# Kernel tuning notes

Measured on AMD Instinct MI355X. Metric: run time of the kernel, lower is better.

The kernel has to match this reference:

```python
import jax, jax.numpy as jnp
import numpy as np

EPS_XVAR = 1e-06
EPS_QVAR = 1e-05
EPS_VAR = 1e-05
MIN_SCALE = 0.1  # rbf kernel
EPS_EDGE = 1e-06


def setup_inputs() -> dict:
    key = jax.random.key(0)
    k1, k2, k3, k4 = jax.random.split(key, 4)
    B, O, I, M = 2048, 64, 64, 32
    x = jax.random.normal(k1, (B, I), dtype=jnp.float32)
    # inducing locations: linspace(-1.5, 1.5, M) tiled over (O, I)
    z = jnp.broadcast_to(jnp.linspace(-1.5, 1.5, M, dtype=jnp.float32), (O, I, M))
    q_mu = jax.random.normal(k2, (O, I, M), dtype=jnp.float32) * 0.05
    q_log_var = jnp.full((O, I, M), -3.0, dtype=jnp.float32)
    log_scale = jnp.zeros((O, I), dtype=jnp.float32)
    log_variance = jnp.full((O, I), -1.0, dtype=jnp.float32)
    return {"x": x, "z": z, "q_mu": q_mu, "q_log_var": q_log_var,
            "log_scale": log_scale, "log_variance": log_variance}


def reference(x, z, q_mu, q_log_var, log_scale, log_variance):
    # x: [B, I]; params: [O, I, M] or [O, I]
    x_mean = x
    x_var = jnp.zeros_like(x) + EPS_XVAR

    q_var = jnp.maximum(jnp.exp(q_log_var), EPS_QVAR)           # [O, I, M]
    var_kern = jnp.maximum(jnp.exp(log_variance), EPS_VAR)      # [O, I]
    lengthscale = jnp.maximum(jnp.exp(log_scale), MIN_SCALE)    # [O, I]

    x_mu_exp = x_mean[:, None, :, None]        # [B, 1, I, 1]
    x_var_exp = x_var[:, None, :, None]        # [B, 1, I, 1]
    ell_sq = (lengthscale ** 2)[None, :, :, None]  # [1, O, I, 1]
    vk = var_kern[None, :, :, None]            # [1, O, I, 1]

    denom = ell_sq + x_var_exp                 # [B, O, I, 1]
    diff = x_mu_exp - z[None]                  # [B, O, I, M]
    psi_1 = vk * jnp.sqrt(ell_sq / denom) * jnp.exp(-0.5 * diff ** 2 / denom)

    edge_means = jnp.sum(psi_1 * q_mu[None], axis=-1)                      # [B, O, I]
    edge_vars = jnp.sum(psi_1 ** 2 * (q_var + q_mu ** 2)[None], axis=-1)   # [B, O, I]
    edge_vars = jnp.maximum(edge_vars - edge_means ** 2, EPS_EDGE)

    return edge_means.sum(axis=2), edge_vars.sum(axis=2)  # each [B, O]
```

## Files before the change

kernel.cpp:

```cpp
#include <hip/hip_runtime.h>

#define BATCH 2048
#define ODIM 64
#define IDIM 64
#define MDIM 32

static constexpr float LOG2E = 1.4426950408889634f;

#if __has_builtin(__builtin_amdgcn_exp2f)
#define EXP2F(x) __builtin_amdgcn_exp2f(x)
#else
#define EXP2F(x) exp2f(x)
#endif

typedef float v2f __attribute__((ext_vector_type(2)));


__global__ __launch_bounds__(256) void prep_kernel(
    const float* __restrict__ z, const float* __restrict__ q_mu,
    const float* __restrict__ q_log_var, const float* __restrict__ log_scale,
    const float* __restrict__ log_variance,
    float4* __restrict__ cmq, float4* __restrict__ aux)
{
    int qt = blockIdx.x * 256 + threadIdx.x;
    int oi = qt >> 4;
    int k  = qt & 15;
    int g  = oi * MDIM + 2 * k;

    float ls   = log_scale[oi];
    float lv   = log_variance[oi];
    float ell  = fmaxf(expf(ls), 0.1f);
    float ell2 = ell * ell;
    float vk   = fmaxf(expf(lv), 1e-5f);
    float denom = ell2 + 1e-6f;
    float A    = vk * sqrtf(ell2 / denom);
    float a    = -0.5f * LOG2E / denom;

    float qm0 = q_mu[g],     qm1 = q_mu[g + 1];
    float qv0 = fmaxf(expf(q_log_var[g]),     1e-5f);
    float qv1 = fmaxf(expf(q_log_var[g + 1]), 1e-5f);
    float zm0 = z[g],        zm1 = z[g + 1];
    float w0  = exp2f(a * zm0 * zm0);
    float w1  = exp2f(a * zm1 * zm1);

    float4 c;
    c.x = A * qm0 * w0;
    c.y = A * A * (qv0 + qm0 * qm0) * w0 * w0;
    c.z = A * qm1 * w1;
    c.w = A * A * (qv1 + qm1 * qm1) * w1 * w1;
    cmq[qt] = c;

    if (k == 0) {
        float z0 = z[oi * MDIM + 0];
        float z1 = z[oi * MDIM + 1];
        float dz = z1 - z0;
        aux[oi] = make_float4(a, -2.0f * a * z0, -2.0f * a * dz, 0.0f);
    }
}

__global__ __launch_bounds__(512, 8) void gpkan_main_kernel(
    const float* __restrict__ x, const float4* __restrict__ cmq,
    const float4* __restrict__ aux, float* __restrict__ out)
{
    const int o     = blockIdx.x & (ODIM - 1);
    const int btile = blockIdx.x >> 6;
    const int tid   = threadIdx.x;
    const int lane  = tid & 63;
    const int wave  = __builtin_amdgcn_readfirstlane(tid >> 6);
    const int b0    = btile * 128 + 2 * lane;
    const int i0    = wave * 8;

    __shared__ float red[2][8][128];

    const float4* pA = (const float4*)(x + (size_t)b0 * IDIM + i0);
    const float4* pB = (const float4*)(x + (size_t)(b0 + 1) * IDIM + i0);
    float4 a0 = pA[0], a1 = pA[1];
    float4 bb0 = pB[0], bb1 = pB[1];

    v2f xv[8];
    xv[0].x = a0.x; xv[0].y = bb0.x;
    xv[1].x = a0.y; xv[1].y = bb0.y;
    xv[2].x = a0.z; xv[2].y = bb0.z;
    xv[3].x = a0.w; xv[3].y = bb0.w;
    xv[4].x = a1.x; xv[4].y = bb1.x;
    xv[5].x = a1.y; xv[5].y = bb1.y;
    xv[6].x = a1.z; xv[6].y = bb1.z;
    xv[7].x = a1.w; xv[7].y = bb1.w;

    const float4* __restrict__ Cb = cmq + ((size_t)o * IDIM + i0) * 16;
    const float4* __restrict__ Ab = aux + o * IDIM + i0;

    v2f emt = {0.f, 0.f};
    v2f evt = {0.f, 0.f};

    #pragma unroll
    for (int ii = 0; ii < 8; ++ii) {
        const float4 Ax = Ab[ii];
        const v2f x2 = xv[ii];

        v2f e1 = {Ax.x, Ax.x}, e2 = {Ax.y, Ax.y}, rc = {Ax.z, Ax.z};

        v2f t = __builtin_elementwise_fma(e1, x2, e2) * x2;
        v2f Eb;
        Eb.x = EXP2F(t.x); Eb.y = EXP2F(t.y);
        v2f ur = rc * x2;
        v2f rr;
        rr.x = EXP2F(ur.x); rr.y = EXP2F(ur.y);

        v2f s = rr * rr;
        v2f u = s * s;

        v2f Pe = {0.f, 0.f}, Po = {0.f, 0.f};
        v2f Qe = {0.f, 0.f}, Qo = {0.f, 0.f};

        const float4* C = Cb + ii * 16;
        #pragma unroll
        for (int k = 15; k >= 0; --k) {
            float4 c = C[k];
            v2f c1e = {c.x, c.x}, c2e = {c.y, c.y};
            v2f c1o = {c.z, c.z}, c2o = {c.w, c.w};
            Pe = __builtin_elementwise_fma(Pe, s, c1e);
            Po = __builtin_elementwise_fma(Po, s, c1o);
            Qe = __builtin_elementwise_fma(Qe, u, c2e);
            Qo = __builtin_elementwise_fma(Qo, u, c2o);
        }

        v2f P = __builtin_elementwise_fma(rr, Po, Pe);
        v2f Q = __builtin_elementwise_fma(s,  Qo, Qe);

        v2f em_i = Eb * P;
        v2f ev_i = (Eb * Eb) * Q;

        v2f eps = {1e-6f, 1e-6f};
        v2f d   = __builtin_elementwise_fma(-em_i, em_i, ev_i);
        evt += __builtin_elementwise_max(d, eps);
        emt += em_i;
    }

    red[0][wave][2 * lane + 0] = emt.x;
    red[0][wave][2 * lane + 1] = emt.y;
    red[1][wave][2 * lane + 0] = evt.x;
    red[1][wave][2 * lane + 1] = evt.y;
    __syncthreads();

    if (tid < 256) {
        const int sel = tid >> 7;
        const int l   = tid & 127;
        float acc = 0.f;
        #pragma unroll
        for (int w = 0; w < 8; ++w) acc += red[sel][w][l];
        const int bb = btile * 128 + l;
        if (sel == 0) out[bb * ODIM + o] = acc;
        else          out[BATCH * ODIM + bb * ODIM + o] = acc;
    }
}

extern "C" void kernel_launch(void* const* d_in, const int* in_sizes, int n_in,
                              void* d_out, int out_size, void* d_ws, size_t ws_size,
                              hipStream_t stream) {
    const float* x            = (const float*)d_in[0];
    const float* z            = (const float*)d_in[1];
    const float* q_mu         = (const float*)d_in[2];
    const float* q_log_var    = (const float*)d_in[3];
    const float* log_scale    = (const float*)d_in[4];
    const float* log_variance = (const float*)d_in[5];
    float* out = (float*)d_out;

    char* ws = (char*)d_ws;
    float4* cmq = (float4*)ws;
    float4* aux = (float4*)(ws + (size_t)ODIM * IDIM * 16 * sizeof(float4));

    prep_kernel<<<dim3(256), dim3(256), 0, stream>>>(
        z, q_mu, q_log_var, log_scale, log_variance, cmq, aux);
    gpkan_main_kernel<<<dim3((BATCH / 128) * ODIM), dim3(512), 0, stream>>>(
        x, cmq, aux, out);
}
```

Before: 81.96 us.

## Fuse parameter prep into main kernel, staging coefficients in LDS

Removes the separate prep kernel and computes the per-(o,i) polynomial coefficients and aux constants inside each main-kernel block, storing them in shared memory. This drops one kernel launch and the workspace round-trip, and the inner loop now reads coefficients from LDS instead of global memory. In exchange, each of the 16 batch tiles per output recomputes the same 64x16 coefficients with expf/exp2 calls. The block also gains about 17 KB of LDS and an extra barrier, which may limit occupancy.

After: 81.75 us. Within noise of the previous version (-0.3%).

```diff
diff --git a/kernel.cpp b/kernel.cpp
--- a/kernel.cpp
+++ b/kernel.cpp
@@ -15,52 +15,11 @@
 
 typedef float v2f __attribute__((ext_vector_type(2)));
 
-
-__global__ __launch_bounds__(256) void prep_kernel(
-    const float* __restrict__ z, const float* __restrict__ q_mu,
-    const float* __restrict__ q_log_var, const float* __restrict__ log_scale,
-    const float* __restrict__ log_variance,
-    float4* __restrict__ cmq, float4* __restrict__ aux)
-{
-    int qt = blockIdx.x * 256 + threadIdx.x;
-    int oi = qt >> 4;
-    int k  = qt & 15;
-    int g  = oi * MDIM + 2 * k;
-
-    float ls   = log_scale[oi];
-    float lv   = log_variance[oi];
-    float ell  = fmaxf(expf(ls), 0.1f);
-    float ell2 = ell * ell;
-    float vk   = fmaxf(expf(lv), 1e-5f);
-    float denom = ell2 + 1e-6f;
-    float A    = vk * sqrtf(ell2 / denom);
-    float a    = -0.5f * LOG2E / denom;
-
-    float qm0 = q_mu[g],     qm1 = q_mu[g + 1];
-    float qv0 = fmaxf(expf(q_log_var[g]),     1e-5f);
-    float qv1 = fmaxf(expf(q_log_var[g + 1]), 1e-5f);
-    float zm0 = z[g],        zm1 = z[g + 1];
-    float w0  = exp2f(a * zm0 * zm0);
-    float w1  = exp2f(a * zm1 * zm1);
-
-    float4 c;
-    c.x = A * qm0 * w0;
-    c.y = A * A * (qv0 + qm0 * qm0) * w0 * w0;
-    c.z = A * qm1 * w1;
-    c.w = A * A * (qv1 + qm1 * qm1) * w1 * w1;
-    cmq[qt] = c;
-
-    if (k == 0) {
-        float z0 = z[oi * MDIM + 0];
-        float z1 = z[oi * MDIM + 1];
-        float dz = z1 - z0;
-        aux[oi] = make_float4(a, -2.0f * a * z0, -2.0f * a * dz, 0.0f);
-    }
-}
-
-__global__ __launch_bounds__(512, 8) void gpkan_main_kernel(
-    const float* __restrict__ x, const float4* __restrict__ cmq,
-    const float4* __restrict__ aux, float* __restrict__ out)
+__global__ __launch_bounds__(512, 8) void gpkan_fused_kernel(
+    const float* __restrict__ x, const float* __restrict__ z,
+    const float* __restrict__ q_mu, const float* __restrict__ q_log_var,
+    const float* __restrict__ log_scale, const float* __restrict__ log_variance,
+    float* __restrict__ out)
 {
     const int o     = blockIdx.x & (ODIM - 1);
     const int btile = blockIdx.x >> 6;
@@ -70,12 +29,52 @@
     const int b0    = btile * 128 + 2 * lane;
     const int i0    = wave * 8;
 
-    __shared__ float red[2][8][128];
+    __shared__ float4 lds_c[IDIM][16];
+    __shared__ float4 lds_aux[IDIM];
+    __shared__ float  red[2][8][128];
 
     const float4* pA = (const float4*)(x + (size_t)b0 * IDIM + i0);
     const float4* pB = (const float4*)(x + (size_t)(b0 + 1) * IDIM + i0);
     float4 a0 = pA[0], a1 = pA[1];
     float4 bb0 = pB[0], bb1 = pB[1];
+
+    #pragma unroll
+    for (int rep = 0; rep < 2; ++rep) {
+        const int q  = tid + rep * 512;
+        const int i  = q >> 4;
+        const int k  = q & 15;
+        const int oi = o * IDIM + i;
+        const int g  = oi * MDIM + 2 * k;
+
+        const float ls = log_scale[oi];
+        const float lv = log_variance[oi];
+        const float ell   = fmaxf(expf(ls), 0.1f);
+        const float ell2  = ell * ell;
+        const float vk    = fmaxf(expf(lv), 1e-5f);
+        const float denom = ell2 + 1e-6f;
+        const float A = vk * sqrtf(ell2 / denom);
+        const float a = -0.5f * LOG2E / denom;
+
+        const float2 qm = *(const float2*)(q_mu + g);
+        const float2 ql = *(const float2*)(q_log_var + g);
+        const float2 zm = *(const float2*)(z + g);
+        const float qv0 = fmaxf(expf(ql.x), 1e-5f);
+        const float qv1 = fmaxf(expf(ql.y), 1e-5f);
+        const float w0  = EXP2F(a * zm.x * zm.x);
+        const float w1  = EXP2F(a * zm.y * zm.y);
+
+        float4 c;
+        c.x = A * qm.x * w0;
+        c.y = A * A * (qv0 + qm.x * qm.x) * w0 * w0;
+        c.z = A * qm.y * w1;
+        c.w = A * A * (qv1 + qm.y * qm.y) * w1 * w1;
+        lds_c[i][k] = c;
+
+        if (k == 0)
+            lds_aux[i] = make_float4(a, -2.0f * a * zm.x,
+                                     -2.0f * a * (zm.y - zm.x), 0.0f);
+    }
+    __syncthreads();
 
     v2f xv[8];
     xv[0].x = a0.x; xv[0].y = bb0.x;
@@ -87,15 +86,12 @@
     xv[6].x = a1.z; xv[6].y = bb1.z;
     xv[7].x = a1.w; xv[7].y = bb1.w;
 
-    const float4* __restrict__ Cb = cmq + ((size_t)o * IDIM + i0) * 16;
-    const float4* __restrict__ Ab = aux + o * IDIM + i0;
-
     v2f emt = {0.f, 0.f};
     v2f evt = {0.f, 0.f};
 
     #pragma unroll
     for (int ii = 0; ii < 8; ++ii) {
-        const float4 Ax = Ab[ii];
+        const float4 Ax = lds_aux[i0 + ii];
         const v2f x2 = xv[ii];
 
         v2f e1 = {Ax.x, Ax.x}, e2 = {Ax.y, Ax.y}, rc = {Ax.z, Ax.z};
@@ -113,7 +109,7 @@
         v2f Pe = {0.f, 0.f}, Po = {0.f, 0.f};
         v2f Qe = {0.f, 0.f}, Qo = {0.f, 0.f};
 
-        const float4* C = Cb + ii * 16;
+        const float4* C = &lds_c[i0 + ii][0];
         #pragma unroll
         for (int k = 15; k >= 0; --k) {
             float4 c = C[k];
@@ -166,12 +162,8 @@
     const float* log_variance = (const float*)d_in[5];
     float* out = (float*)d_out;
 
-    char* ws = (char*)d_ws;
-    float4* cmq = (float4*)ws;
-    float4* aux = (float4*)(ws + (size_t)ODIM * IDIM * 16 * sizeof(float4));
+    (void)d_ws; (void)ws_size;
 
-    prep_kernel<<<dim3(256), dim3(256), 0, stream>>>(
-        z, q_mu, q_log_var, log_scale, log_variance, cmq, aux);
-    gpkan_main_kernel<<<dim3((BATCH / 128) * ODIM), dim3(512), 0, stream>>>(
-        x, cmq, aux, out);
+    gpkan_fused_kernel<<<dim3((BATCH / 128) * ODIM), dim3(512), 0, stream>>>(
+        x, z, q_mu, q_log_var, log_scale, log_variance, out);
 }
```
